# Optimization experiments

Measured on AMD Instinct MI355X. Metric: run time of the kernel, lower is better.

Reference implementation:

```python
import jax, jax.numpy as jnp
import numpy as np

DIM = 4096
N_HEADS = 32
N_KV = 8
HEAD_DIM = DIM // N_HEADS  # 128
ROPE_THETA = 10000.0


def setup_inputs() -> dict:
    key = jax.random.key(0)
    ks = jax.random.split(key, 5)
    B, S = 1, 2048
    x = jax.random.normal(ks[0], (B, S, DIM), jnp.float32)
    wq = jax.random.normal(ks[1], (N_HEADS * HEAD_DIM, DIM), jnp.float32) * 0.02
    wk = jax.random.normal(ks[2], (N_KV * HEAD_DIM, DIM), jnp.float32) * 0.02
    wv = jax.random.normal(ks[3], (N_KV * HEAD_DIM, DIM), jnp.float32) * 0.02
    wo = jax.random.normal(ks[4], (DIM, DIM), jnp.float32) * 0.02
    # precomputed RoPE frequencies: angle[t, i] = t / theta^(2i/head_dim)
    inv_freq = 1.0 / (ROPE_THETA ** (jnp.arange(0, HEAD_DIM, 2, dtype=jnp.float32) / HEAD_DIM))
    t = jnp.arange(S, dtype=jnp.float32)
    angles = jnp.outer(t, inv_freq)  # [S, HEAD_DIM/2]
    return {"x": x, "wq": wq, "wk": wk, "wv": wv, "wo": wo,
            "freqs_cos": jnp.cos(angles), "freqs_sin": jnp.sin(angles)}


def _apply_rope(v, cos, sin):
    # v: [B, S, H, HEAD_DIM]; cos/sin: [S, HEAD_DIM/2]
    # mirrors torch view_as_complex on (..., hd/2, 2): even idx = real, odd idx = imag
    vr = v.reshape(*v.shape[:-1], HEAD_DIM // 2, 2)
    xr, xi = vr[..., 0], vr[..., 1]
    c = cos[None, :, None, :]
    s = sin[None, :, None, :]
    out_r = xr * c - xi * s
    out_i = xr * s + xi * c
    return jnp.stack([out_r, out_i], axis=-1).reshape(v.shape)


def reference(x, wq, wk, wv, wo, freqs_cos, freqs_sin):
    B, S, _ = x.shape
    rep = N_HEADS // N_KV
    q = (x @ wq.T).reshape(B, S, N_HEADS, HEAD_DIM)
    k = (x @ wk.T).reshape(B, S, N_KV, HEAD_DIM)
    v = (x @ wv.T).reshape(B, S, N_KV, HEAD_DIM)
    q = _apply_rope(q, freqs_cos, freqs_sin)
    k = _apply_rope(k, freqs_cos, freqs_sin)
    # native GQA: group query heads per kv head instead of materializing repeated KV
    qg = q.reshape(B, S, N_KV, rep, HEAD_DIM)
    scale = 1.0 / jnp.sqrt(jnp.asarray(HEAD_DIM, jnp.float32))
    scores = jnp.einsum('bqkrd,bskd->bkrqs', qg, k) * scale  # [B, n_kv, rep, S, S]
    causal = jnp.tril(jnp.ones((S, S), bool))
    scores = jnp.where(causal, scores, -jnp.inf)
    probs = jax.nn.softmax(scores, axis=-1)
    out = jnp.einsum('bkrqs,bskd->bqkrd', probs, v).reshape(B, S, DIM)
    return out @ wo.T
```

## Files before the change

kernel.cpp:

```cpp
#include <hip/hip_runtime.h>
#include <cstdint>

typedef __attribute__((ext_vector_type(8))) __bf16 bf16x8;
typedef __attribute__((ext_vector_type(4))) float  f32x4;
typedef __attribute__((ext_vector_type(8))) unsigned short ushort8;

#define DIM 4096
#define SEQ 2048
#define NH  32
#define NKV 8
#define HD  128

__device__ __forceinline__ float b2f(unsigned short u) {
  union { unsigned int i; float f; } v; v.i = ((unsigned int)u) << 16; return v.f;
}
__device__ __forceinline__ unsigned short f2b(float f) {
  union { float f; unsigned int i; } v; v.f = f;
  unsigned int r = v.i + 0x7fffu + ((v.i >> 16) & 1u);
  return (unsigned short)(r >> 16);
}

__device__ __forceinline__ void gl_lds16(const void* g, void* l) {
  __builtin_amdgcn_global_load_lds(
      (const __attribute__((address_space(1))) void*)(uintptr_t)g,
      (__attribute__((address_space(3))) void*)(uintptr_t)l,
      16, 0, 0);
}

__global__ __launch_bounds__(256) void f32_to_bf16(const float* __restrict__ src,
                                                   unsigned short* __restrict__ dst, int n) {
  const int i = (blockIdx.x * 256 + threadIdx.x) * 8;
  if (i >= n) return;
  const float4 a = *(const float4*)(src + i);
  const float4 b = *(const float4*)(src + i + 4);
  ushort8 o;
  o[0] = f2b(a.x); o[1] = f2b(a.y); o[2] = f2b(a.z); o[3] = f2b(a.w);
  o[4] = f2b(b.x); o[5] = f2b(b.y); o[6] = f2b(b.z); o[7] = f2b(b.w);
  *(ushort8*)(dst + i) = o;
}

template <bool OUT_F32>
__global__ __launch_bounds__(256) void gemm_bt(const unsigned short* __restrict__ A,
                                               const unsigned short* __restrict__ B,
                                               void* __restrict__ Cv,
                                               int M, int N, int K) {
  __shared__ __align__(16) unsigned short As[128 * 32];
  __shared__ __align__(16) unsigned short Bs[128 * 32];
  const int n0   = blockIdx.x * 128;
  const int m0   = blockIdx.y * 128;
  const int tid  = threadIdx.x;
  const int w    = tid >> 6;
  const int lane = tid & 63;
  const int quad = lane >> 4;
  const int l15  = lane & 15;
  const int wm   = (w & 1) * 64;
  const int wn   = (w >> 1) * 64;

  const f32x4 fzero = {0.f, 0.f, 0.f, 0.f};
  f32x4 acc[4][4];
#pragma unroll
  for (int i = 0; i < 4; ++i)
#pragma unroll
    for (int j = 0; j < 4; ++j) acc[i][j] = fzero;

  const int srow = lane >> 2;
  const int scol = (lane & 3) * 8;

  for (int k0 = 0; k0 < K; k0 += 32) {
    __syncthreads();
#pragma unroll
    for (int cc = 0; cc < 2; ++cc) {
      const int c   = w * 2 + cc;
      const int row = c * 16 + srow;
      gl_lds16(A + (size_t)(m0 + row) * K + k0 + scol, (char*)As + c * 1024);
      gl_lds16(B + (size_t)(n0 + row) * K + k0 + scol, (char*)Bs + c * 1024);
    }
    __syncthreads();

    bf16x8 af[4], bfr[4];
#pragma unroll
    for (int i = 0; i < 4; ++i) {
      af[i]  = *(const bf16x8*)(As + (wm + i * 16 + l15) * 32 + quad * 8);
      bfr[i] = *(const bf16x8*)(Bs + (wn + i * 16 + l15) * 32 + quad * 8);
    }
#pragma unroll
    for (int i = 0; i < 4; ++i)
#pragma unroll
      for (int j = 0; j < 4; ++j)
        acc[i][j] = __builtin_amdgcn_mfma_f32_16x16x32_bf16(af[i], bfr[j], acc[i][j], 0, 0, 0);
  }

#pragma unroll
  for (int i = 0; i < 4; ++i)
#pragma unroll
    for (int j = 0; j < 4; ++j) {
      const int m = m0 + wm + i * 16 + quad * 4;
      const int n = n0 + wn + j * 16 + l15;
      if (OUT_F32) {
        float* cp = (float*)Cv + (size_t)m * N + n;
#pragma unroll
        for (int r = 0; r < 4; ++r) cp[(size_t)r * N] = acc[i][j][r];
      } else {
        unsigned short* cp = (unsigned short*)Cv + (size_t)m * N + n;
#pragma unroll
        for (int r = 0; r < 4; ++r) cp[(size_t)r * N] = f2b(acc[i][j][r]);
      }
    }
}

__global__ void rope_kernel(unsigned short* __restrict__ q, int qstride,
                            unsigned short* __restrict__ k, int kstride,
                            const float* __restrict__ Ct, const float* __restrict__ St) {
  const int idx = blockIdx.x * 256 + threadIdx.x;
  const int total = SEQ * (NH * 64 + NKV * 64);
  if (idx >= total) return;
  const int s = idx / 2560;
  const int r = idx - s * 2560;
  unsigned short* base;
  int i;
  if (r < NH * 64) {
    const int h = r >> 6; i = r & 63;
    base = q + (size_t)s * qstride + h * HD + 2 * i;
  } else {
    const int r2 = r - NH * 64; const int h = r2 >> 6; i = r2 & 63;
    base = k + (size_t)s * kstride + h * HD + 2 * i;
  }
  const float c  = Ct[s * 64 + i];
  const float sn = St[s * 64 + i];
  const float xr = b2f(base[0]);
  const float xi = b2f(base[1]);
  base[0] = f2b(xr * c - xi * sn);
  base[1] = f2b(xr * sn + xi * c);
}

__global__ __launch_bounds__(256) void transpose_v(const unsigned short* __restrict__ v,
                                                   int vstride,
                                                   unsigned short* __restrict__ vt) {
  __shared__ unsigned short tile[64][72];
  const int bs = blockIdx.x;
  const int bd = blockIdx.y;
  const int t  = threadIdx.x;
  const int r  = t >> 2;
  const int c0 = (t & 3) * 16;
  const unsigned short* src = v + (size_t)(bs * 64 + r) * vstride + bd * 64 + c0;
#pragma unroll
  for (int i = 0; i < 2; ++i) {
    ushort8 d = *(const ushort8*)(src + i * 8);
#pragma unroll
    for (int e = 0; e < 8; ++e) tile[r][c0 + i * 8 + e] = d[e];
  }
  __syncthreads();
  unsigned short* dst = vt + (size_t)(bd * 64 + r) * SEQ + bs * 64 + c0;
#pragma unroll
  for (int i = 0; i < 2; ++i) {
    ushort8 o;
#pragma unroll
    for (int e = 0; e < 8; ++e) o[e] = tile[c0 + i * 8 + e][r];
    *(ushort8*)(dst + i * 8) = o;
  }
}

__global__ __launch_bounds__(256) void attn_kernel(const unsigned short* __restrict__ Q, int qstride,
                                                   const unsigned short* __restrict__ K, int kstride,
                                                   const unsigned short* __restrict__ VT,
                                                   unsigned short* __restrict__ O) {
  const int bid  = blockIdx.x;
  const int h    = bid & 31;
  const int pr   = bid >> 5;
  const int g    = h >> 2;
  const int tid  = threadIdx.x;
  const int w    = tid >> 6;
  const int lane = tid & 63;
  const int quad = lane >> 4;
  const int l15  = lane & 15;

  __shared__ __align__(16) unsigned short Ks[64 * 128];
  __shared__ __align__(16) unsigned short Vs[128 * 64];
  __shared__ __align__(16) unsigned short Ps[4][32 * 64];

  const float scale = 0.08838834764831845f;
  const f32x4 fzero = {0.f, 0.f, 0.f, 0.f};

  bf16x8 onesf;
#pragma unroll
  for (int e = 0; e < 8; ++e) onesf[e] = (__bf16)1.0f;

  const int ks_row = (lane >> 4);
  const int ks_q   = (lane & 15);
  const int vs_row = (lane >> 3);
  const int vs_q   = (lane & 7) ^ (lane >> 3);

  unsigned short* pw = Ps[w];

  for (int phase = 0; phase < 2; ++phase) {
    const int qt    = phase ? (15 - pr) : pr;
    const int qrow0 = qt * 128 + w * 32;

    bf16x8 qf[2][4];
#pragma unroll
    for (int gq = 0; gq < 2; ++gq) {
      const unsigned short* qb = Q + (size_t)(qrow0 + gq * 16 + l15) * qstride + h * HD + quad * 8;
#pragma unroll
      for (int c = 0; c < 4; ++c) qf[gq][c] = *(const bf16x8*)(qb + c * 32);
    }

    f32x4 oa[2][8];
    f32x4 ls[2];
#pragma unroll
    for (int gq = 0; gq < 2; ++gq) {
      ls[gq] = fzero;
#pragma unroll
      for (int i = 0; i < 8; ++i) oa[gq][i] = fzero;
    }

    const int n_tiles = 2 * qt + 2;

    for (int kt = 0; kt < n_tiles; ++kt) {
      const int kv0 = kt * 64;
      __syncthreads();
#pragma unroll
      for (int cc = 0; cc < 4; ++cc) {
        const int c = w * 4 + cc;
        {
          const int row = c * 4 + ks_row;
          const int qch = ks_q ^ (row & 15);
          gl_lds16(K + (size_t)(kv0 + row) * kstride + g * HD + qch * 8, (char*)Ks + c * 1024);
        }
        {
          const int row = c * 8 + vs_row;
          gl_lds16(VT + (size_t)(g * HD + row) * SEQ + kv0 + vs_q * 8, (char*)Vs + c * 1024);
        }
      }
      __syncthreads();

      f32x4 s[2][4];
#pragma unroll
      for (int gq = 0; gq < 2; ++gq)
#pragma unroll
        for (int ks = 0; ks < 4; ++ks) s[gq][ks] = fzero;
#pragma unroll
      for (int c = 0; c < 4; ++c)
#pragma unroll
        for (int ks = 0; ks < 4; ++ks) {
          const int row = ks * 16 + l15;
          const int p   = (c * 4 + quad) ^ l15;
          bf16x8 kf = *(const bf16x8*)(Ks + row * 128 + p * 8);
          s[0][ks] = __builtin_amdgcn_mfma_f32_16x16x32_bf16(qf[0][c], kf, s[0][ks], 0, 0, 0);
          s[1][ks] = __builtin_amdgcn_mfma_f32_16x16x32_bf16(qf[1][c], kf, s[1][ks], 0, 0, 0);
        }

#pragma unroll
      for (int gq = 0; gq < 2; ++gq)
#pragma unroll
        for (int r = 0; r < 4; ++r) {
          const int qrow = qrow0 + gq * 16 + quad * 4 + r;
          const int prow = gq * 16 + quad * 4 + r;
#pragma unroll
          for (int ks = 0; ks < 4; ++ks) {
            const float ex = __expf(s[gq][ks][r] * scale);
            const float e  = (kv0 + ks * 16 + l15 <= qrow) ? ex : 0.f;
            const int qc = ks * 2 + (l15 >> 3);
            const int p  = qc ^ (prow & 7);
            pw[prow * 64 + p * 8 + (l15 & 7)] = f2b(e);
          }
        }

#pragma unroll
      for (int ki = 0; ki < 2; ++ki) {
        bf16x8 pf[2];
#pragma unroll
        for (int gq = 0; gq < 2; ++gq) {
          const int row = gq * 16 + l15;
          const int p   = (ki * 4 + quad) ^ (l15 & 7);
          pf[gq] = *(const bf16x8*)(pw + row * 64 + p * 8);
        }
        ls[0] = __builtin_amdgcn_mfma_f32_16x16x32_bf16(pf[0], onesf, ls[0], 0, 0, 0);
        ls[1] = __builtin_amdgcn_mfma_f32_16x16x32_bf16(pf[1], onesf, ls[1], 0, 0, 0);
#pragma unroll
        for (int nt = 0; nt < 8; ++nt) {
          const int vrow = nt * 16 + l15;
          const int p    = (ki * 4 + quad) ^ (l15 & 7);
          bf16x8 vf = *(const bf16x8*)(Vs + vrow * 64 + p * 8);
          oa[0][nt] = __builtin_amdgcn_mfma_f32_16x16x32_bf16(pf[0], vf, oa[0][nt], 0, 0, 0);
          oa[1][nt] = __builtin_amdgcn_mfma_f32_16x16x32_bf16(pf[1], vf, oa[1][nt], 0, 0, 0);
        }
      }
    }

#pragma unroll
    for (int gq = 0; gq < 2; ++gq)
#pragma unroll
      for (int r = 0; r < 4; ++r) {
        const float inv = 1.f / ls[gq][r];
        const int qrow = qrow0 + gq * 16 + quad * 4 + r;
        unsigned short* orow = O + (size_t)qrow * DIM + h * HD;
#pragma unroll
        for (int nt = 0; nt < 8; ++nt) orow[nt * 16 + l15] = f2b(oa[gq][nt][r] * inv);
      }
  }
}

extern "C" void kernel_launch(void* const* d_in, const int* in_sizes, int n_in,
                              void* d_out, int out_size, void* d_ws, size_t ws_size,
                              hipStream_t stream) {
  const float* x  = (const float*)d_in[0];
  const float* wq = (const float*)d_in[1];
  const float* wk = (const float*)d_in[2];
  const float* wv = (const float*)d_in[3];
  const float* wo = (const float*)d_in[4];
  const float* fc = (const float*)d_in[5];
  const float* fs = (const float*)d_in[6];
  float* outp = (float*)d_out;

  const dim3 blk(256);
  const size_t M1 = 1024 * 1024;
  const int nx  = SEQ * DIM;
  const int nqw = DIM * DIM;
  const int nkw = NKV * HD * DIM;
  const int total = SEQ * (NH * 64 + NKV * 64);

  const size_t fused_elems = (8 + 24 + 12 + 2 + 8) * M1;

  if (ws_size >= fused_elems * 2) {
    unsigned short* xb   = (unsigned short*)d_ws;
    unsigned short* wbuf = xb   + 8  * M1;
    unsigned short* qkv  = wbuf + 24 * M1;
    unsigned short* vtb  = qkv  + 12 * M1;
    unsigned short* aob  = vtb  + 2  * M1;

    f32_to_bf16<<<dim3(nx  / 2048), blk, 0, stream>>>(x,  xb, nx);
    f32_to_bf16<<<dim3(nqw / 2048), blk, 0, stream>>>(wq, wbuf, nqw);
    f32_to_bf16<<<dim3(nkw / 2048), blk, 0, stream>>>(wk, wbuf + 16 * M1, nkw);
    f32_to_bf16<<<dim3(nkw / 2048), blk, 0, stream>>>(wv, wbuf + 20 * M1, nkw);

    gemm_bt<false><<<dim3(6144 / 128, SEQ / 128), blk, 0, stream>>>(xb, wbuf, qkv, SEQ, 6144, DIM);

    rope_kernel<<<dim3((total + 255) / 256), blk, 0, stream>>>(qkv, 6144, qkv + 4096, 6144, fc, fs);
    transpose_v<<<dim3(SEQ / 64, 1024 / 64), blk, 0, stream>>>(qkv + 5120, 6144, vtb);
    attn_kernel<<<dim3(256), blk, 0, stream>>>(qkv, 6144, qkv + 4096, 6144, vtb, aob);

    f32_to_bf16<<<dim3(nqw / 2048), blk, 0, stream>>>(wo, wbuf, nqw);
    gemm_bt<true><<<dim3(DIM / 128, SEQ / 128), blk, 0, stream>>>(aob, wbuf, outp, SEQ, DIM, DIM);
  } else {
    unsigned short* xb   = (unsigned short*)d_ws;
    unsigned short* wbuf = xb   + 8  * M1;
    unsigned short* qb   = wbuf + 16 * M1;
    unsigned short* kvb  = qb   + 8  * M1;
    unsigned short* vtb  = kvb  + 4  * M1;
    unsigned short* aob  = vtb  + 2  * M1;

    f32_to_bf16<<<dim3(nx  / 2048), blk, 0, stream>>>(x,  xb, nx);
    f32_to_bf16<<<dim3(nqw / 2048), blk, 0, stream>>>(wq, wbuf, nqw);
    gemm_bt<false><<<dim3(DIM / 128, SEQ / 128), blk, 0, stream>>>(xb, wbuf, qb, SEQ, DIM, DIM);

    f32_to_bf16<<<dim3(nkw / 2048), blk, 0, stream>>>(wk, wbuf, nkw);
    f32_to_bf16<<<dim3(nkw / 2048), blk, 0, stream>>>(wv, wbuf + 4 * M1, nkw);
    gemm_bt<false><<<dim3(2048 / 128, SEQ / 128), blk, 0, stream>>>(xb, wbuf, kvb, SEQ, 2048, DIM);

    rope_kernel<<<dim3((total + 255) / 256), blk, 0, stream>>>(qb, 4096, kvb, 2048, fc, fs);
    transpose_v<<<dim3(SEQ / 64, 1024 / 64), blk, 0, stream>>>(kvb + 1024, 2048, vtb);
    attn_kernel<<<dim3(256), blk, 0, stream>>>(qb, 4096, kvb, 2048, vtb, aob);

    f32_to_bf16<<<dim3(nqw / 2048), blk, 0, stream>>>(wo, wbuf, nqw);
    gemm_bt<true><<<dim3(DIM / 128, SEQ / 128), blk, 0, stream>>>(aob, wbuf, outp, SEQ, DIM, DIM);
  }
}
```

Before: 539.7 us.

## Add 256x256-tile double-buffered GEMM kernel for fused QKV projection

Introduces a new 512-thread GEMM with 256x256 output tiles, XOR-swizzled LDS staging via direct global-to-LDS loads, two-stage prefetch, and MFMA work split around the next tile's load issue. It replaces the 128x128 GEMM for the fused QKV projection only. Larger tiles raise operand reuse per LDS load, but the grid shrinks to 24x8=192 blocks, which may underfill the GPU's compute units, and the register and LDS demand per block rises.

```diff
diff --git a/kernel.cpp b/kernel.cpp
--- a/kernel.cpp
+++ b/kernel.cpp
@@ -108,6 +108,128 @@
     }
 }
 
+template <bool OUT_F32>
+__global__ __launch_bounds__(512, 2) void gemm256(const unsigned short* __restrict__ A,
+                                                  const unsigned short* __restrict__ B,
+                                                  void* __restrict__ Cv,
+                                                  int M, int N, int K) {
+  __shared__ __align__(16) unsigned short As[2][256 * 64];
+  __shared__ __align__(16) unsigned short Bs[2][256 * 64];
+
+  const int n0   = blockIdx.x * 256;
+  const int m0   = blockIdx.y * 256;
+  const int tid  = threadIdx.x;
+  const int w    = tid >> 6;
+  const int lane = tid & 63;
+  const int quad = lane >> 4;
+  const int l15  = lane & 15;
+  const int wm   = (w >> 2) * 128;
+  const int wn   = (w & 3) * 64;
+
+  const int srow = lane >> 3;
+  const int sgr  = (lane & 7) ^ srow;
+  const unsigned short* aS = A + (size_t)(m0 + srow) * K + sgr * 8;
+  const unsigned short* bS = B + (size_t)(n0 + srow) * K + sgr * 8;
+
+  const int gr0 = ((quad)     ^ (l15 & 7)) * 8;
+  const int gr1 = ((quad + 4) ^ (l15 & 7)) * 8;
+
+  const f32x4 fzero = {0.f, 0.f, 0.f, 0.f};
+  f32x4 acc[8][4];
+#pragma unroll
+  for (int i = 0; i < 8; ++i)
+#pragma unroll
+    for (int j = 0; j < 4; ++j) acc[i][j] = fzero;
+
+  const int NT = K >> 6;
+
+#pragma unroll
+  for (int tp = 0; tp < 2; ++tp)
+#pragma unroll
+    for (int i = 0; i < 4; ++i) {
+      const int c = w * 4 + i;
+      gl_lds16(aS + (size_t)c * 8 * K + tp * 64, (char*)As[tp] + c * 1024);
+      gl_lds16(bS + (size_t)c * 8 * K + tp * 64, (char*)Bs[tp] + c * 1024);
+    }
+
+  for (int t = 0; t < NT; ++t) {
+    const unsigned short* Ab = As[t & 1] + (wm + l15) * 64;
+    const unsigned short* Bb = Bs[t & 1] + (wn + l15) * 64;
+
+    if (t + 2 < NT) asm volatile("s_waitcnt vmcnt(8)" ::: "memory");
+    else            asm volatile("s_waitcnt vmcnt(0)" ::: "memory");
+    __builtin_amdgcn_s_barrier();
+    __builtin_amdgcn_sched_barrier(0);
+
+    bf16x8 af[8][2], bfr[4][2];
+#pragma unroll
+    for (int mf = 0; mf < 8; ++mf) {
+      af[mf][0] = *(const bf16x8*)(Ab + mf * 1024 + gr0);
+      af[mf][1] = *(const bf16x8*)(Ab + mf * 1024 + gr1);
+    }
+#pragma unroll
+    for (int nf = 0; nf < 4; ++nf) {
+      bfr[nf][0] = *(const bf16x8*)(Bb + nf * 1024 + gr0);
+      bfr[nf][1] = *(const bf16x8*)(Bb + nf * 1024 + gr1);
+    }
+
+    __builtin_amdgcn_s_setprio(1);
+#pragma unroll
+    for (int ks = 0; ks < 2; ++ks)
+#pragma unroll
+      for (int mf = 0; mf < 4; ++mf)
+#pragma unroll
+        for (int nf = 0; nf < 4; ++nf)
+          acc[mf][nf] = __builtin_amdgcn_mfma_f32_16x16x32_bf16(af[mf][ks], bfr[nf][ks],
+                                                                acc[mf][nf], 0, 0, 0);
+    __builtin_amdgcn_s_setprio(0);
+
+    asm volatile("s_waitcnt lgkmcnt(0)" ::: "memory");
+    __builtin_amdgcn_sched_barrier(0);
+    __builtin_amdgcn_s_barrier();
+
+    if (t + 2 < NT) {
+      const int koff = (t + 2) * 64;
+      unsigned short* Ad = As[t & 1];
+      unsigned short* Bd = Bs[t & 1];
+#pragma unroll
+      for (int i = 0; i < 4; ++i) {
+        const int c = w * 4 + i;
+        gl_lds16(aS + (size_t)c * 8 * K + koff, (char*)Ad + c * 1024);
+        gl_lds16(bS + (size_t)c * 8 * K + koff, (char*)Bd + c * 1024);
+      }
+    }
+
+    __builtin_amdgcn_s_setprio(1);
+#pragma unroll
+    for (int ks = 0; ks < 2; ++ks)
+#pragma unroll
+      for (int mf = 4; mf < 8; ++mf)
+#pragma unroll
+        for (int nf = 0; nf < 4; ++nf)
+          acc[mf][nf] = __builtin_amdgcn_mfma_f32_16x16x32_bf16(af[mf][ks], bfr[nf][ks],
+                                                                acc[mf][nf], 0, 0, 0);
+    __builtin_amdgcn_s_setprio(0);
+  }
+
+#pragma unroll
+  for (int mf = 0; mf < 8; ++mf)
+#pragma unroll
+    for (int nf = 0; nf < 4; ++nf) {
+      const int m = m0 + wm + mf * 16 + quad * 4;
+      const int n = n0 + wn + nf * 16 + l15;
+      if (OUT_F32) {
+        float* cp = (float*)Cv + (size_t)m * N + n;
+#pragma unroll
+        for (int r = 0; r < 4; ++r) cp[(size_t)r * N] = acc[mf][nf][r];
+      } else {
+        unsigned short* cp = (unsigned short*)Cv + (size_t)m * N + n;
+#pragma unroll
+        for (int r = 0; r < 4; ++r) cp[(size_t)r * N] = f2b(acc[mf][nf][r]);
+      }
+    }
+}
+
 __global__ void rope_kernel(unsigned short* __restrict__ q, int qstride,
                             unsigned short* __restrict__ k, int kstride,
                             const float* __restrict__ Ct, const float* __restrict__ St) {
@@ -333,7 +455,8 @@
     f32_to_bf16<<<dim3(nkw / 2048), blk, 0, stream>>>(wk, wbuf + 16 * M1, nkw);
     f32_to_bf16<<<dim3(nkw / 2048), blk, 0, stream>>>(wv, wbuf + 20 * M1, nkw);
 
-    gemm_bt<false><<<dim3(6144 / 128, SEQ / 128), blk, 0, stream>>>(xb, wbuf, qkv, SEQ, 6144, DIM);
+    gemm256<false><<<dim3(6144 / 256, SEQ / 256), dim3(512), 0, stream>>>(xb, wbuf, qkv,
+                                                                          SEQ, 6144, DIM);
 
     rope_kernel<<<dim3((total + 255) / 256), blk, 0, stream>>>(qkv, 6144, qkv + 4096, 6144, fc, fs);
     transpose_v<<<dim3(SEQ / 64, 1024 / 64), blk, 0, stream>>>(qkv + 5120, 6144, vtb);
```

Result: faster. 516.7 us (-4.3%).
